# Kernel tuning notes

Hardware: AMD Instinct MI355X
Metric: run time of the kernel (lower is better)

## Reference

```python
import jax, jax.numpy as jnp
import numpy as np

B, S, D = 32, 2048, 128
SCALE = 11.313708498984761  # sqrt(128)


def setup_inputs() -> dict:
    key = jax.random.key(0)
    kq, kk, kv = jax.random.split(key, 3)
    q = jax.random.normal(kq, (B, S, D), dtype=jnp.float32)
    k = jax.random.normal(kk, (B, S, D), dtype=jnp.float32)
    v = jax.random.normal(kv, (B, S, D), dtype=jnp.float32)
    # causal mask: True where masked (j > i), broadcast across batch
    causal = jnp.triu(jnp.ones((S, S), dtype=bool), k=1)
    mask = jnp.broadcast_to(causal, (B, S, S))
    return {"q": q, "k": k, "v": v, "mask": mask}


def reference(q, k, v, mask):
    # a = (q @ k^T) / scale, masked_fill(mask, -inf), softmax over keys, a @ v
    a = jnp.einsum("bqd,bkd->bqk", q, k) / SCALE  # [B, S, S]
    a = jnp.where(mask, -jnp.inf, a)
    a = jax.nn.softmax(a, axis=2)
    output = jnp.einsum("bqk,bkd->bqd", a, v)  # [B, S, D]
    return (a, output)
```

## Files before the change

kernel.cpp:

```cpp
#include <hip/hip_runtime.h>
#include <hip/hip_bf16.h>
#include <math.h>


typedef __attribute__((ext_vector_type(8))) short bf16x8;
typedef __attribute__((ext_vector_type(4))) short bf16x4;
typedef __attribute__((ext_vector_type(4))) float f32x4;

#define MFMA(a, b, c) __builtin_amdgcn_mfma_f32_16x16x32_bf16((a), (b), (c), 0, 0, 0)

constexpr int   Sdim  = 2048;
constexpr int   Ddim  = 128;
constexpr int   BATCH = 32;
constexpr int   NT    = Sdim / 64;
constexpr float INV_SCALE = 0.08838834764831845f;
constexpr float NEG_BIG   = -1e30f;
constexpr int   KPAD = 8;
constexpr int   PADV = 8;
constexpr int   PADP = 8;

__device__ __forceinline__ void bar_lds() {
    asm volatile("s_waitcnt lgkmcnt(0)\n\ts_barrier" ::: "memory");
}

__device__ __forceinline__ bf16x8 pack8(const float* p) {
    float4 a = *(const float4*)p;
    float4 b = *(const float4*)(p + 4);
    union { __hip_bfloat16 h[8]; bf16x8 v; } u;
    u.h[0] = __float2bfloat16(a.x); u.h[1] = __float2bfloat16(a.y);
    u.h[2] = __float2bfloat16(a.z); u.h[3] = __float2bfloat16(a.w);
    u.h[4] = __float2bfloat16(b.x); u.h[5] = __float2bfloat16(b.y);
    u.h[6] = __float2bfloat16(b.z); u.h[7] = __float2bfloat16(b.w);
    return u.v;
}

__device__ __forceinline__ bf16x4 pack4(float4 a) {
    union { __hip_bfloat16 h[4]; bf16x4 v; } u;
    u.h[0] = __float2bfloat16(a.x); u.h[1] = __float2bfloat16(a.y);
    u.h[2] = __float2bfloat16(a.z); u.h[3] = __float2bfloat16(a.w);
    return u.v;
}

__global__ __launch_bounds__(256, 2)
void attn_kernel(const float* __restrict__ qg,
                 const float* __restrict__ kg,
                 const float* __restrict__ vg,
                 float* __restrict__ a_out,
                 float* __restrict__ o_out)
{
    const int flat = blockIdx.x;
    const int xcd  = flat & 7;
    const int rdec = flat >> 3;
    const int jb   = rdec & 15;
    const int b    = xcd + 8 * (rdec >> 4);

    const int tid  = threadIdx.x;
    const int wave = tid >> 6;
    const int lane = tid & 63;
    const int li   = lane & 15;
    const int quad = lane >> 4;

    __shared__ __hip_bfloat16 kl[64][Ddim + KPAD];
    __shared__ __hip_bfloat16 vt[Ddim][64 + PADV];
    __shared__ __hip_bfloat16 pt[64][64 + PADP];

    const size_t boff = (size_t)b * Sdim * Ddim;
    const float* qb = qg + boff;
    const float* kb = kg + boff;
    const float* vb = vg + boff;
    float* ab = a_out + (size_t)b * Sdim * Sdim;

    int skk[8], sd0[8];
    #pragma unroll
    for (int it = 0; it < 8; ++it) {
        const int idx = tid + it * 256;
        skk[it] = idx >> 5;
        sd0[it] = (idx & 31) * 4;
    }

    for (int sel = 0; sel < 2; ++sel) {
        const int qi   = sel ? (NT - 1 - jb) : jb;
        const int q0   = qi * 64;
        const int row0 = q0 + wave * 16;

        bf16x8 qf[4];
        {
            const float* qrow = qb + (size_t)(row0 + li) * Ddim + quad * 8;
            #pragma unroll
            for (int ks = 0; ks < 4; ++ks)
                qf[ks] = pack8(qrow + ks * 32);
        }

        {
            const int c0  = (qi + 1) * 64;
            const int zc4 = (Sdim - c0) >> 2;
            const f32x4 z = (f32x4){0.f, 0.f, 0.f, 0.f};
            for (int rr = 0; rr < 16; ++rr) {
                f32x4* dst = (f32x4*)(ab + (size_t)(row0 + rr) * Sdim + c0);
                for (int c = lane; c < zc4; c += 64)
                    __builtin_nontemporal_store(z, dst + c);
            }
        }

        float m[4], l[4];
        #pragma unroll
        for (int r = 0; r < 4; ++r) { m[r] = NEG_BIG; l[r] = 0.f; }

        float4 kpre[8];
        #pragma unroll
        for (int it = 0; it < 8; ++it)
            kpre[it] = *(const float4*)(kb + (size_t)skk[it] * Ddim + sd0[it]);

        for (int kt = 0; kt <= qi; ++kt) {
            bar_lds();
            #pragma unroll
            for (int it = 0; it < 8; ++it)
                *(bf16x4*)&kl[skk[it]][sd0[it]] = pack4(kpre[it]);
            bar_lds();

            if (kt < qi) {
                const float* kbt = kb + (size_t)(kt + 1) * 64 * Ddim;
                #pragma unroll
                for (int it = 0; it < 8; ++it)
                    kpre[it] = *(const float4*)(kbt + (size_t)skk[it] * Ddim + sd0[it]);
            }

            const int kv0 = kt * 64;
            f32x4 acc[4];
            #pragma unroll
            for (int t = 0; t < 4; ++t) acc[t] = (f32x4){0.f, 0.f, 0.f, 0.f};
            __builtin_amdgcn_s_setprio(1);
            #pragma unroll
            for (int t = 0; t < 4; ++t)
                #pragma unroll
                for (int ks = 0; ks < 4; ++ks) {
                    bf16x8 kf = *(const bf16x8*)&kl[t * 16 + li][ks * 32 + quad * 8];
                    acc[t] = MFMA(qf[ks], kf, acc[t]);
                }
            __builtin_amdgcn_s_setprio(0);

            float s[4][4];
            #pragma unroll
            for (int t = 0; t < 4; ++t)
                #pragma unroll
                for (int r = 0; r < 4; ++r) {
                    float sv = acc[t][r] * INV_SCALE;
                    if (kt == qi) {
                        int col = kv0 + t * 16 + li;
                        int row = row0 + quad * 4 + r;
                        if (col > row) sv = NEG_BIG;
                    }
                    s[t][r] = sv;
                }

            #pragma unroll
            for (int r = 0; r < 4; ++r) {
                float tm = fmaxf(fmaxf(s[0][r], s[1][r]), fmaxf(s[2][r], s[3][r]));
                #pragma unroll
                for (int off = 1; off < 16; off <<= 1)
                    tm = fmaxf(tm, __shfl_xor(tm, off, 64));
                float mn    = fmaxf(m[r], tm);
                float alpha = __expf(m[r] - mn);
                float se = __expf(s[0][r] - mn) + __expf(s[1][r] - mn)
                         + __expf(s[2][r] - mn) + __expf(s[3][r] - mn);
                #pragma unroll
                for (int off = 1; off < 16; off <<= 1)
                    se += __shfl_xor(se, off, 64);
                l[r] = l[r] * alpha + se;
                m[r] = mn;
            }
        }

        float invl[4];
        #pragma unroll
        for (int r = 0; r < 4; ++r) invl[r] = 1.0f / l[r];

        f32x4 oacc[8];
        #pragma unroll
        for (int n = 0; n < 8; ++n) oacc[n] = (f32x4){0.f, 0.f, 0.f, 0.f};

        float4 vpre[8];
        #pragma unroll
        for (int it = 0; it < 8; ++it) {
            kpre[it] = *(const float4*)(kb + (size_t)skk[it] * Ddim + sd0[it]);
            vpre[it] = *(const float4*)(vb + (size_t)skk[it] * Ddim + sd0[it]);
        }

        for (int kt = 0; kt <= qi; ++kt) {
            const int kv0 = kt * 64;

            bar_lds();
            #pragma unroll
            for (int it = 0; it < 8; ++it)
                *(bf16x4*)&kl[skk[it]][sd0[it]] = pack4(kpre[it]);
            #pragma unroll
            for (int it = 0; it < 8; ++it) {
                const int kk = skk[it], d0 = sd0[it];
                float4 vv = vpre[it];
                vt[d0 + 0][kk] = __float2bfloat16(vv.x);
                vt[d0 + 1][kk] = __float2bfloat16(vv.y);
                vt[d0 + 2][kk] = __float2bfloat16(vv.z);
                vt[d0 + 3][kk] = __float2bfloat16(vv.w);
            }
            bar_lds();

            if (kt < qi) {
                const float* kbt = kb + (size_t)(kt + 1) * 64 * Ddim;
                const float* vbt = vb + (size_t)(kt + 1) * 64 * Ddim;
                #pragma unroll
                for (int it = 0; it < 8; ++it) {
                    kpre[it] = *(const float4*)(kbt + (size_t)skk[it] * Ddim + sd0[it]);
                    vpre[it] = *(const float4*)(vbt + (size_t)skk[it] * Ddim + sd0[it]);
                }
            }

            f32x4 acc[4];
            #pragma unroll
            for (int t = 0; t < 4; ++t) acc[t] = (f32x4){0.f, 0.f, 0.f, 0.f};
            __builtin_amdgcn_s_setprio(1);
            #pragma unroll
            for (int t = 0; t < 4; ++t)
                #pragma unroll
                for (int ks = 0; ks < 4; ++ks) {
                    bf16x8 kf = *(const bf16x8*)&kl[t * 16 + li][ks * 32 + quad * 8];
                    acc[t] = MFMA(qf[ks], kf, acc[t]);
                }
            __builtin_amdgcn_s_setprio(0);

            #pragma unroll
            for (int r = 0; r < 4; ++r) {
                const int rowL = wave * 16 + quad * 4 + r;
                float* dst = ab + (size_t)(q0 + rowL) * Sdim + kv0 + li;
                #pragma unroll
                for (int t = 0; t < 4; ++t) {
                    float sv = acc[t][r] * INV_SCALE;
                    if (kt == qi && (kv0 + t * 16 + li) > (q0 + rowL)) sv = NEG_BIG;
                    float p = __expf(sv - m[r]) * invl[r];
                    pt[rowL][t * 16 + li] = __float2bfloat16(p);
                    __builtin_nontemporal_store(p, dst + t * 16);
                }
            }

            asm volatile("s_waitcnt lgkmcnt(0)" ::: "memory");

            __builtin_amdgcn_s_setprio(1);
            #pragma unroll
            for (int ks = 0; ks < 2; ++ks) {
                bf16x8 pf = *(const bf16x8*)&pt[wave * 16 + li][ks * 32 + quad * 8];
                #pragma unroll
                for (int nt = 0; nt < 8; ++nt) {
                    bf16x8 vf = *(const bf16x8*)&vt[nt * 16 + li][ks * 32 + quad * 8];
                    oacc[nt] = MFMA(pf, vf, oacc[nt]);
                }
            }
            __builtin_amdgcn_s_setprio(0);
        }

        float* ob = o_out + ((size_t)b * Sdim + row0) * Ddim;
        #pragma unroll
        for (int n = 0; n < 8; ++n)
            #pragma unroll
            for (int r = 0; r < 4; ++r)
                __builtin_nontemporal_store(oacc[n][r],
                    ob + (size_t)(quad * 4 + r) * Ddim + n * 16 + li);
    }
}

extern "C" void kernel_launch(void* const* d_in, const int* in_sizes, int n_in,
                              void* d_out, int out_size, void* d_ws, size_t ws_size,
                              hipStream_t stream)
{
    const float* q = (const float*)d_in[0];
    const float* k = (const float*)d_in[1];
    const float* v = (const float*)d_in[2];

    float* a = (float*)d_out;
    float* o = a + (size_t)BATCH * Sdim * Sdim;

    attn_kernel<<<dim3(512), 256, 0, stream>>>(q, k, v, a, o);
}
```

Before: 1.043 ms.

## Compute softmax statistics with transposed MFMA from global K, swizzle V transpose in LDS

The first pass, which computes row max and sum, now loads K straight from global memory into MFMA operands with no LDS staging or barriers. It also swaps the MFMA operand order so each lane holds one query row's scores, which cuts the per-row shuffle reductions to two xor-shuffles. The per-row statistics are then broadcast to the layout the second pass needs. Separately, the transposed V tile in LDS gets an XOR swizzle on its column index to reduce bank conflicts on the scattered bf16 writes and the vector reads. The risk is that the first pass now makes uncoalesced direct global K reads per wave that rely on cache reuse.

```diff
diff --git a/kernel.cpp b/kernel.cpp
--- a/kernel.cpp
+++ b/kernel.cpp
@@ -102,30 +102,103 @@
             }
         }
 
-        float m[4], l[4];
-        #pragma unroll
-        for (int r = 0; r < 4; ++r) { m[r] = NEG_BIG; l[r] = 0.f; }
-
-        float4 kpre[8];
-        #pragma unroll
-        for (int it = 0; it < 8; ++it)
+        float m_s = NEG_BIG, l_s = 0.f;
+
+        for (int kt = 0; kt <= qi; ++kt) {
+            const int kv0 = kt * 64;
+
+            f32x4 acc[4];
+            #pragma unroll
+            for (int t = 0; t < 4; ++t) acc[t] = (f32x4){0.f, 0.f, 0.f, 0.f};
+
+            #pragma unroll
+            for (int t = 0; t < 4; ++t) {
+                const float* kp = kb + (size_t)(kv0 + t * 16 + li) * Ddim + quad * 8;
+                #pragma unroll
+                for (int ks = 0; ks < 4; ++ks) {
+                    bf16x8 kf = pack8(kp + ks * 32);
+                    acc[t] = MFMA(kf, qf[ks], acc[t]);
+                }
+            }
+
+            float s[4][4];
+            float tm = NEG_BIG;
+            #pragma unroll
+            for (int t = 0; t < 4; ++t)
+                #pragma unroll
+                for (int r = 0; r < 4; ++r) {
+                    float sv = acc[t][r] * INV_SCALE;
+                    if (kt == qi) {
+                        if ((t * 16 + quad * 4 + r) > (wave * 16 + li)) sv = NEG_BIG;
+                    }
+                    s[t][r] = sv;
+                    tm = fmaxf(tm, sv);
+                }
+            tm = fmaxf(tm, __shfl_xor(tm, 16, 64));
+            tm = fmaxf(tm, __shfl_xor(tm, 32, 64));
+
+            float mn    = fmaxf(m_s, tm);
+            float alpha = __expf(m_s - mn);
+            float se = 0.f;
+            #pragma unroll
+            for (int t = 0; t < 4; ++t)
+                #pragma unroll
+                for (int r = 0; r < 4; ++r)
+                    se += __expf(s[t][r] - mn);
+            se += __shfl_xor(se, 16, 64);
+            se += __shfl_xor(se, 32, 64);
+            l_s = l_s * alpha + se;
+            m_s = mn;
+        }
+
+        const float invl_s = 1.0f / l_s;
+        float m_r[4], invl_r[4];
+        #pragma unroll
+        for (int r = 0; r < 4; ++r) {
+            m_r[r]    = __shfl(m_s,    quad * 4 + r, 64);
+            invl_r[r] = __shfl(invl_s, quad * 4 + r, 64);
+        }
+
+        f32x4 oacc[8];
+        #pragma unroll
+        for (int n = 0; n < 8; ++n) oacc[n] = (f32x4){0.f, 0.f, 0.f, 0.f};
+
+        float4 kpre[8], vpre[8];
+        #pragma unroll
+        for (int it = 0; it < 8; ++it) {
             kpre[it] = *(const float4*)(kb + (size_t)skk[it] * Ddim + sd0[it]);
+            vpre[it] = *(const float4*)(vb + (size_t)skk[it] * Ddim + sd0[it]);
+        }
 
         for (int kt = 0; kt <= qi; ++kt) {
+            const int kv0 = kt * 64;
+
             bar_lds();
             #pragma unroll
             for (int it = 0; it < 8; ++it)
                 *(bf16x4*)&kl[skk[it]][sd0[it]] = pack4(kpre[it]);
+            #pragma unroll
+            for (int it = 0; it < 8; ++it) {
+                const int kk = skk[it], d0 = sd0[it];
+                const int cp = (((kk >> 3) ^ ((d0 >> 2) & 7)) << 3) | (kk & 7);
+                float4 vv = vpre[it];
+                vt[d0 + 0][cp] = __float2bfloat16(vv.x);
+                vt[d0 + 1][cp] = __float2bfloat16(vv.y);
+                vt[d0 + 2][cp] = __float2bfloat16(vv.z);
+                vt[d0 + 3][cp] = __float2bfloat16(vv.w);
+            }
             bar_lds();
 
             if (kt < qi) {
                 const float* kbt = kb + (size_t)(kt + 1) * 64 * Ddim;
-                #pragma unroll
-                for (int it = 0; it < 8; ++it)
+                const float* vbt = vb + (size_t)(kt + 1) * 64 * Ddim;
+                #pragma unroll
+                for (int it = 0; it < 8; ++it) {
                     kpre[it] = *(const float4*)(kbt + (size_t)skk[it] * Ddim + sd0[it]);
-            }
-
-            const int kv0 = kt * 64;
+                    vpre[it] = *(const float4*)(vbt + (size_t)skk[it] * Ddim + sd0[it]);
+                }
+            }
+
             f32x4 acc[4];
             #pragma unroll
             for (int t = 0; t < 4; ++t) acc[t] = (f32x4){0.f, 0.f, 0.f, 0.f};
@@ -139,94 +212,6 @@
                 }
             __builtin_amdgcn_s_setprio(0);
 
-            float s[4][4];
-            #pragma unroll
-            for (int t = 0; t < 4; ++t)
-                #pragma unroll
-                for (int r = 0; r < 4; ++r) {
-                    float sv = acc[t][r] * INV_SCALE;
-                    if (kt == qi) {
-                        int col = kv0 + t * 16 + li;
-                        int row = row0 + quad * 4 + r;
-                        if (col > row) sv = NEG_BIG;
-                    }
-                    s[t][r] = sv;
-                }
-
-            #pragma unroll
-            for (int r = 0; r < 4; ++r) {
-                float tm = fmaxf(fmaxf(s[0][r], s[1][r]), fmaxf(s[2][r], s[3][r]));
-                #pragma unroll
-                for (int off = 1; off < 16; off <<= 1)
-                    tm = fmaxf(tm, __shfl_xor(tm, off, 64));
-                float mn    = fmaxf(m[r], tm);
-                float alpha = __expf(m[r] - mn);
-                float se = __expf(s[0][r] - mn) + __expf(s[1][r] - mn)
-                         + __expf(s[2][r] - mn) + __expf(s[3][r] - mn);
-                #pragma unroll
-                for (int off = 1; off < 16; off <<= 1)
-                    se += __shfl_xor(se, off, 64);
-                l[r] = l[r] * alpha + se;
-                m[r] = mn;
-            }
-        }
-
-        float invl[4];
-        #pragma unroll
-        for (int r = 0; r < 4; ++r) invl[r] = 1.0f / l[r];
-
-        f32x4 oacc[8];
-        #pragma unroll
-        for (int n = 0; n < 8; ++n) oacc[n] = (f32x4){0.f, 0.f, 0.f, 0.f};
-
-        float4 vpre[8];
-        #pragma unroll
-        for (int it = 0; it < 8; ++it) {
-            kpre[it] = *(const float4*)(kb + (size_t)skk[it] * Ddim + sd0[it]);
-            vpre[it] = *(const float4*)(vb + (size_t)skk[it] * Ddim + sd0[it]);
-        }
-
-        for (int kt = 0; kt <= qi; ++kt) {
-            const int kv0 = kt * 64;
-
-            bar_lds();
-            #pragma unroll
-            for (int it = 0; it < 8; ++it)
-                *(bf16x4*)&kl[skk[it]][sd0[it]] = pack4(kpre[it]);
-            #pragma unroll
-            for (int it = 0; it < 8; ++it) {
-                const int kk = skk[it], d0 = sd0[it];
-                float4 vv = vpre[it];
-                vt[d0 + 0][kk] = __float2bfloat16(vv.x);
-                vt[d0 + 1][kk] = __float2bfloat16(vv.y);
-                vt[d0 + 2][kk] = __float2bfloat16(vv.z);
-                vt[d0 + 3][kk] = __float2bfloat16(vv.w);
-            }
-            bar_lds();
-
-            if (kt < qi) {
-                const float* kbt = kb + (size_t)(kt + 1) * 64 * Ddim;
-                const float* vbt = vb + (size_t)(kt + 1) * 64 * Ddim;
-                #pragma unroll
-                for (int it = 0; it < 8; ++it) {
-                    kpre[it] = *(const float4*)(kbt + (size_t)skk[it] * Ddim + sd0[it]);
-                    vpre[it] = *(const float4*)(vbt + (size_t)skk[it] * Ddim + sd0[it]);
-                }
-            }
-
-            f32x4 acc[4];
-            #pragma unroll
-            for (int t = 0; t < 4; ++t) acc[t] = (f32x4){0.f, 0.f, 0.f, 0.f};
-            __builtin_amdgcn_s_setprio(1);
-            #pragma unroll
-            for (int t = 0; t < 4; ++t)
-                #pragma unroll
-                for (int ks = 0; ks < 4; ++ks) {
-                    bf16x8 kf = *(const bf16x8*)&kl[t * 16 + li][ks * 32 + quad * 8];
-                    acc[t] = MFMA(qf[ks], kf, acc[t]);
-                }
-            __builtin_amdgcn_s_setprio(0);
-
             #pragma unroll
             for (int r = 0; r < 4; ++r) {
                 const int rowL = wave * 16 + quad * 4 + r;
@@ -235,7 +220,7 @@
                 for (int t = 0; t < 4; ++t) {
                     float sv = acc[t][r] * INV_SCALE;
                     if (kt == qi && (kv0 + t * 16 + li) > (q0 + rowL)) sv = NEG_BIG;
-                    float p = __expf(sv - m[r]) * invl[r];
+                    float p = __expf(sv - m_r[r]) * invl_r[r];
                     pt[rowL][t * 16 + li] = __float2bfloat16(p);
                     __builtin_nontemporal_store(p, dst + t * 16);
                 }
@@ -249,7 +234,10 @@
                 bf16x8 pf = *(const bf16x8*)&pt[wave * 16 + li][ks * 32 + quad * 8];
                 #pragma unroll
                 for (int nt = 0; nt < 8; ++nt) {
-                    bf16x8 vf = *(const bf16x8*)&vt[nt * 16 + li][ks * 32 + quad * 8];
+                    const int row = nt * 16 + li;
+                    const int g   = (row >> 2) & 7;
+                    const int cb  = (((ks * 4 + quad) ^ g) << 3);
+                    bf16x8 vf = *(const bf16x8*)&vt[row][cb];
                     oacc[nt] = MFMA(pf, vf, oacc[nt]);
                 }
             }
```

Measured after the change: 1.238 ms. 1.19x slower.
